# Kernel optimization log

Measured on AMD Instinct MI355X. Metric: run time of the kernel, lower is better.

## Reference

```python
import jax, jax.numpy as jnp
import numpy as np

N = 32768        # tokens (batch*seq)
D = 1024         # input_dim
E = 64           # n_experts
TOPK = 2


def setup_inputs() -> dict:
    key = jax.random.key(0)
    k_x, k_w, k_b, k_wn, k_bn = jax.random.split(key, 5)
    scale = 1.0 / np.sqrt(D)
    return {
        "x": jax.random.normal(k_x, (N, D), dtype=jnp.float32),
        "W": jax.random.uniform(k_w, (D, E), minval=-scale, maxval=scale, dtype=jnp.float32),
        "b": jax.random.uniform(k_b, (E,), minval=-scale, maxval=scale, dtype=jnp.float32),
        "W_noise": jax.random.uniform(k_wn, (D, E), minval=-scale, maxval=scale, dtype=jnp.float32),
        "b_noise": jax.random.uniform(k_bn, (E,), minval=-scale, maxval=scale, dtype=jnp.float32),
    }


def reference(x, W, b, W_noise, b_noise):
    # logits = fc(x): single Linear (router_hidden_dims=[])
    logits = x @ W + b                      # [N, E]
    # training=False (default): no noise path; fc_noise params unused
    topk_logits, topk_indices = jax.lax.top_k(logits, TOPK)  # [N, k]
    # scatter topk logits into a -inf tensor, then softmax
    mask = jnp.sum(jax.nn.one_hot(topk_indices, E, dtype=jnp.bool_), axis=-2)  # [N, E]
    sparse_logits = jnp.where(mask, logits, -jnp.inf)
    routing_probs = jax.nn.softmax(sparse_logits, axis=-1)  # zeros off-topk
    return routing_probs, topk_indices
```

## Files before the change

kernel.cpp:

```cpp
#include <hip/hip_runtime.h>
#include <cstdint>
#include <cstddef>

#define N_TOK 32768
#define DIM   1024
#define NE    64
#define BM    64
#define BK    32
#define NTILES (DIM / BK)

__device__ __forceinline__ void gload16(const float* g, float* l) {
  __builtin_amdgcn_global_load_lds(
      (const __attribute__((address_space(1))) uint32_t*)g,
      (__attribute__((address_space(3))) uint32_t*)l, 16, 0, 0);
}

__global__ __launch_bounds__(256, 2) void router_kernel(
    const float* __restrict__ x, const float* __restrict__ W,
    const float* __restrict__ bias, float* __restrict__ probs,
    float* __restrict__ idxo) {
  __shared__ __align__(1024) float lds[2][4096];

  const int tid  = threadIdx.x;
  const int lane = tid & 63;
  const int wv   = __builtin_amdgcn_readfirstlane(tid >> 6);
  const int tx   = tid & 15;
  const int ty   = tid >> 4;
  const int r0   = blockIdx.x * BM;

  auto stage = [&](int t, int b) {
    const int d0 = t * BK;
    float* xl = &lds[b][0];
    float* wl = &lds[b][2048];
#pragma unroll
    for (int q = 0; q < 2; ++q) {
      const int s = (wv * 2 + q) * 64 + lane;
      gload16(W + (size_t)d0 * NE + (size_t)s * 4, wl + (wv * 2 + q) * 256);
      const int row = s >> 3;
      const int g   = s & 7;
      gload16(x + (size_t)(r0 + row) * DIM + d0 + ((g ^ (row & 7)) << 2),
              xl + (wv * 2 + q) * 256);
    }
  };

  float4 acc[4];
#pragma unroll
  for (int i = 0; i < 4; ++i) acc[i] = make_float4(0.f, 0.f, 0.f, 0.f);

  stage(0, 0);

  for (int t = 0; t < NTILES; ++t) {
    const int b = t & 1;
    __syncthreads();
    if (t + 1 < NTILES) stage(t + 1, (t + 1) & 1);

    const float* wl = &lds[b][2048];
    uintptr_t xb[4];
#pragma unroll
    for (int i = 0; i < 4; ++i) {
      const int r = 4 * ty + i;
      xb[i] = (uintptr_t)(&lds[b][0]) + (uintptr_t)r * (BK * 4) + (uintptr_t)((r & 7) << 4);
    }

#pragma unroll
    for (int q = 0; q < 8; ++q) {
      float4 a0 = *(const float4*)(xb[0] ^ (uintptr_t)(q << 4));
      float4 a1 = *(const float4*)(xb[1] ^ (uintptr_t)(q << 4));
      float4 a2 = *(const float4*)(xb[2] ^ (uintptr_t)(q << 4));
      float4 a3 = *(const float4*)(xb[3] ^ (uintptr_t)(q << 4));
      float4 b0 = *(const float4*)(wl + (q * 4 + 0) * NE + tx * 4);
      float4 b1 = *(const float4*)(wl + (q * 4 + 1) * NE + tx * 4);
      float4 b2 = *(const float4*)(wl + (q * 4 + 2) * NE + tx * 4);
      float4 b3 = *(const float4*)(wl + (q * 4 + 3) * NE + tx * 4);

#define ROWFMA(ACC, A)                                                        \
      ACC.x = fmaf(A.x, b0.x, ACC.x); ACC.y = fmaf(A.x, b0.y, ACC.y);         \
      ACC.z = fmaf(A.x, b0.z, ACC.z); ACC.w = fmaf(A.x, b0.w, ACC.w);         \
      ACC.x = fmaf(A.y, b1.x, ACC.x); ACC.y = fmaf(A.y, b1.y, ACC.y);         \
      ACC.z = fmaf(A.y, b1.z, ACC.z); ACC.w = fmaf(A.y, b1.w, ACC.w);         \
      ACC.x = fmaf(A.z, b2.x, ACC.x); ACC.y = fmaf(A.z, b2.y, ACC.y);         \
      ACC.z = fmaf(A.z, b2.z, ACC.z); ACC.w = fmaf(A.z, b2.w, ACC.w);         \
      ACC.x = fmaf(A.w, b3.x, ACC.x); ACC.y = fmaf(A.w, b3.y, ACC.y);         \
      ACC.z = fmaf(A.w, b3.z, ACC.z); ACC.w = fmaf(A.w, b3.w, ACC.w);

      ROWFMA(acc[0], a0)
      ROWFMA(acc[1], a1)
      ROWFMA(acc[2], a2)
      ROWFMA(acc[3], a3)
#undef ROWFMA
    }
  }

  const float4 bv = *(const float4*)(bias + tx * 4);
#pragma unroll
  for (int i = 0; i < 4; ++i) {
    float4 l = acc[i];
    l.x += bv.x; l.y += bv.y; l.z += bv.z; l.w += bv.w;

    float v1, v2; int j1, j2;
    if (l.y > l.x) { v1 = l.y; j1 = 1; v2 = l.x; j2 = 0; }
    else           { v1 = l.x; j1 = 0; v2 = l.y; j2 = 1; }
    if (l.z > v1)      { v2 = v1; j2 = j1; v1 = l.z; j1 = 2; }
    else if (l.z > v2) { v2 = l.z; j2 = 2; }
    if (l.w > v1)      { v2 = v1; j2 = j1; v1 = l.w; j1 = 3; }
    else if (l.w > v2) { v2 = l.w; j2 = 3; }
    j1 += tx * 4; j2 += tx * 4;

#pragma unroll
    for (int m = 8; m >= 1; m >>= 1) {
      float u1 = __shfl_xor(v1, m, 64);
      int   k1 = __shfl_xor(j1, m, 64);
      float u2 = __shfl_xor(v2, m, 64);
      int   k2 = __shfl_xor(j2, m, 64);
      bool firstWins = (u1 > v1) || (u1 == v1 && k1 < j1);
      if (firstWins) {
        bool u2b = (u2 > v1) || (u2 == v1 && k2 < j1);
        v2 = u2b ? u2 : v1; j2 = u2b ? k2 : j1;
        v1 = u1; j1 = k1;
      } else if ((u1 > v2) || (u1 == v2 && k1 < j2)) {
        v2 = u1; j2 = k1;
      }
    }

    const float e2v = __expf(v2 - v1);
    const float inv = 1.0f / (1.0f + e2v);
    const float p1 = inv, p2 = e2v * inv;

    const int row = r0 + 4 * ty + i;
    const int e0  = tx * 4;
    float4 o;
    o.x = (e0 + 0 == j1) ? p1 : (e0 + 0 == j2) ? p2 : 0.0f;
    o.y = (e0 + 1 == j1) ? p1 : (e0 + 1 == j2) ? p2 : 0.0f;
    o.z = (e0 + 2 == j1) ? p1 : (e0 + 2 == j2) ? p2 : 0.0f;
    o.w = (e0 + 3 == j1) ? p1 : (e0 + 3 == j2) ? p2 : 0.0f;
    *(float4*)(probs + (size_t)row * NE + e0) = o;

    if (tx == 0) {
      float2 oi; oi.x = (float)j1; oi.y = (float)j2;
      *(float2*)(idxo + (size_t)row * 2) = oi;
    }
  }
}

extern "C" void kernel_launch(void* const* d_in, const int* in_sizes, int n_in,
                              void* d_out, int out_size, void* d_ws, size_t ws_size,
                              hipStream_t stream) {
  (void)in_sizes; (void)n_in; (void)out_size; (void)d_ws; (void)ws_size;
  const float* x = (const float*)d_in[0];
  const float* W = (const float*)d_in[1];
  const float* b = (const float*)d_in[2];
  float* out  = (float*)d_out;
  float* idxo = out + (size_t)N_TOK * NE;

  dim3 grid(N_TOK / BM);
  dim3 block(256);
  hipLaunchKernelGGL(router_kernel, grid, block, 0, stream, x, W, b, out, idxo);
}
```

Before: 254.2 us.

## Split K across wave halves, read W via scalar loads, reduce partials in LDS

```diff
diff --git a/kernel.cpp b/kernel.cpp
--- a/kernel.cpp
+++ b/kernel.cpp
@@ -5,9 +5,10 @@
 #define N_TOK 32768
 #define DIM   1024
 #define NE    64
-#define BM    64
-#define BK    32
-#define NTILES (DIM / BK)
+#define RPB   64
+#define KHALF 512
+#define CHUNK 32
+#define NCHUNK (KHALF / CHUNK)
 
 __device__ __forceinline__ void gload16(const float* g, float* l) {
   __builtin_amdgcn_global_load_lds(
@@ -15,129 +16,131 @@
       (__attribute__((address_space(3))) uint32_t*)l, 16, 0, 0);
 }
 
-__global__ __launch_bounds__(256, 2) void router_kernel(
+__global__ __launch_bounds__(512, 4) void router_kernel(
     const float* __restrict__ x, const float* __restrict__ W,
     const float* __restrict__ bias, float* __restrict__ probs,
     float* __restrict__ idxo) {
-  __shared__ __align__(1024) float lds[2][4096];
+  __shared__ __align__(1024) float xs[2][2][RPB][CHUNK];
+  __shared__ float  red[4][RPB][16];
+  __shared__ float4 ex[4][RPB];
+  __shared__ float4 ex2[RPB];
 
   const int tid  = threadIdx.x;
   const int lane = tid & 63;
-  const int wv   = __builtin_amdgcn_readfirstlane(tid >> 6);
-  const int tx   = tid & 15;
-  const int ty   = tid >> 4;
-  const int r0   = blockIdx.x * BM;
+  const int w    = __builtin_amdgcn_readfirstlane(tid >> 6);
+  const int g    = w & 3;
+  const int h    = w >> 2;
+  const int r0   = blockIdx.x * RPB;
 
-  auto stage = [&](int t, int b) {
-    const int d0 = t * BK;
-    float* xl = &lds[b][0];
-    float* wl = &lds[b][2048];
+  auto stage = [&](int cc) {
+    const int buf = cc & 1;
+    float* base = &xs[h][buf][0][0];
+    const int k0 = h * KHALF + cc * CHUNK;
 #pragma unroll
-    for (int q = 0; q < 2; ++q) {
-      const int s = (wv * 2 + q) * 64 + lane;
-      gload16(W + (size_t)d0 * NE + (size_t)s * 4, wl + (wv * 2 + q) * 256);
-      const int row = s >> 3;
-      const int g   = s & 7;
-      gload16(x + (size_t)(r0 + row) * DIM + d0 + ((g ^ (row & 7)) << 2),
-              xl + (wv * 2 + q) * 256);
+    for (int jj = 0; jj < 2; ++jj) {
+      const int j = 2 * g + jj;
+      const int row = 8 * j + (lane >> 3);
+      const int sq  = (lane & 7) ^ (lane >> 3);
+      gload16(x + (size_t)(r0 + row) * DIM + k0 + (sq << 2),
+              base + j * 256);
     }
   };
 
-  float4 acc[4];
+  float acc[16];
 #pragma unroll
-  for (int i = 0; i < 4; ++i) acc[i] = make_float4(0.f, 0.f, 0.f, 0.f);
+  for (int e = 0; e < 16; ++e) acc[e] = 0.0f;
 
-  stage(0, 0);
+  stage(0);
 
-  for (int t = 0; t < NTILES; ++t) {
-    const int b = t & 1;
+  for (int cc = 0; cc < NCHUNK; ++cc) {
     __syncthreads();
-    if (t + 1 < NTILES) stage(t + 1, (t + 1) & 1);
+    if (cc + 1 < NCHUNK) stage(cc + 1);
 
-    const float* wl = &lds[b][2048];
-    uintptr_t xb[4];
+    const int buf = cc & 1;
+    const float* xb = &xs[h][buf][0][0] + lane * CHUNK;
+    const float* Wc = W + (size_t)(h * KHALF + cc * CHUNK) * NE + g * 16;
+
+    float4 xq = make_float4(0.f, 0.f, 0.f, 0.f);
 #pragma unroll
-    for (int i = 0; i < 4; ++i) {
-      const int r = 4 * ty + i;
-      xb[i] = (uintptr_t)(&lds[b][0]) + (uintptr_t)r * (BK * 4) + (uintptr_t)((r & 7) << 4);
-    }
-
+    for (int kk = 0; kk < CHUNK; ++kk) {
+      if ((kk & 3) == 0) {
+        const int slot = (kk >> 2) ^ (lane & 7);
+        xq = *(const float4*)(xb + (slot << 2));
+      }
+      const float xc = ((kk & 3) == 0) ? xq.x
+                     : ((kk & 3) == 1) ? xq.y
+                     : ((kk & 3) == 2) ? xq.z : xq.w;
+      const float* Wk = Wc + (size_t)kk * NE;
 #pragma unroll
-    for (int q = 0; q < 8; ++q) {
-      float4 a0 = *(const float4*)(xb[0] ^ (uintptr_t)(q << 4));
-      float4 a1 = *(const float4*)(xb[1] ^ (uintptr_t)(q << 4));
-      float4 a2 = *(const float4*)(xb[2] ^ (uintptr_t)(q << 4));
-      float4 a3 = *(const float4*)(xb[3] ^ (uintptr_t)(q << 4));
-      float4 b0 = *(const float4*)(wl + (q * 4 + 0) * NE + tx * 4);
-      float4 b1 = *(const float4*)(wl + (q * 4 + 1) * NE + tx * 4);
-      float4 b2 = *(const float4*)(wl + (q * 4 + 2) * NE + tx * 4);
-      float4 b3 = *(const float4*)(wl + (q * 4 + 3) * NE + tx * 4);
-
-#define ROWFMA(ACC, A)                                                        \
-      ACC.x = fmaf(A.x, b0.x, ACC.x); ACC.y = fmaf(A.x, b0.y, ACC.y);         \
-      ACC.z = fmaf(A.x, b0.z, ACC.z); ACC.w = fmaf(A.x, b0.w, ACC.w);         \
-      ACC.x = fmaf(A.y, b1.x, ACC.x); ACC.y = fmaf(A.y, b1.y, ACC.y);         \
-      ACC.z = fmaf(A.y, b1.z, ACC.z); ACC.w = fmaf(A.y, b1.w, ACC.w);         \
-      ACC.x = fmaf(A.z, b2.x, ACC.x); ACC.y = fmaf(A.z, b2.y, ACC.y);         \
-      ACC.z = fmaf(A.z, b2.z, ACC.z); ACC.w = fmaf(A.z, b2.w, ACC.w);         \
-      ACC.x = fmaf(A.w, b3.x, ACC.x); ACC.y = fmaf(A.w, b3.y, ACC.y);         \
-      ACC.z = fmaf(A.w, b3.z, ACC.z); ACC.w = fmaf(A.w, b3.w, ACC.w);
-
-      ROWFMA(acc[0], a0)
-      ROWFMA(acc[1], a1)
-      ROWFMA(acc[2], a2)
-      ROWFMA(acc[3], a3)
-#undef ROWFMA
+      for (int e = 0; e < 16; ++e)
+        acc[e] = fmaf(Wk[e], xc, acc[e]);
     }
   }
 
-  const float4 bv = *(const float4*)(bias + tx * 4);
+  __syncthreads();
+  if (h == 1) {
 #pragma unroll
-  for (int i = 0; i < 4; ++i) {
-    float4 l = acc[i];
-    l.x += bv.x; l.y += bv.y; l.z += bv.z; l.w += bv.w;
+    for (int q = 0; q < 4; ++q)
+      *(float4*)&red[g][lane][q * 4] = make_float4(acc[q*4+0], acc[q*4+1],
+                                                   acc[q*4+2], acc[q*4+3]);
+  }
+  __syncthreads();
+
+  if (h == 0) {
+#pragma unroll
+    for (int q = 0; q < 4; ++q) {
+      float4 r = *(const float4*)&red[g][lane][q * 4];
+      acc[q*4+0] += r.x; acc[q*4+1] += r.y; acc[q*4+2] += r.z; acc[q*4+3] += r.w;
+    }
+#pragma unroll
+    for (int e = 0; e < 16; ++e) acc[e] += bias[g * 16 + e];
 
     float v1, v2; int j1, j2;
-    if (l.y > l.x) { v1 = l.y; j1 = 1; v2 = l.x; j2 = 0; }
-    else           { v1 = l.x; j1 = 0; v2 = l.y; j2 = 1; }
-    if (l.z > v1)      { v2 = v1; j2 = j1; v1 = l.z; j1 = 2; }
-    else if (l.z > v2) { v2 = l.z; j2 = 2; }
-    if (l.w > v1)      { v2 = v1; j2 = j1; v1 = l.w; j1 = 3; }
-    else if (l.w > v2) { v2 = l.w; j2 = 3; }
-    j1 += tx * 4; j2 += tx * 4;
+    if (acc[1] > acc[0]) { v1 = acc[1]; j1 = 1; v2 = acc[0]; j2 = 0; }
+    else                 { v1 = acc[0]; j1 = 0; v2 = acc[1]; j2 = 1; }
+#pragma unroll
+    for (int e = 2; e < 16; ++e) {
+      if (acc[e] > v1)      { v2 = v1; j2 = j1; v1 = acc[e]; j1 = e; }
+      else if (acc[e] > v2) { v2 = acc[e]; j2 = e; }
+    }
+    ex[g][lane] = make_float4(v1, v2, (float)(g * 16 + j1), (float)(g * 16 + j2));
+  }
+  __syncthreads();
 
+  if (w == 0) {
+    float4 m = ex[0][lane];
+    float V1 = m.x, V2 = m.y, J1 = m.z, J2 = m.w;
 #pragma unroll
-    for (int m = 8; m >= 1; m >>= 1) {
-      float u1 = __shfl_xor(v1, m, 64);
-      int   k1 = __shfl_xor(j1, m, 64);
-      float u2 = __shfl_xor(v2, m, 64);
-      int   k2 = __shfl_xor(j2, m, 64);
-      bool firstWins = (u1 > v1) || (u1 == v1 && k1 < j1);
-      if (firstWins) {
-        bool u2b = (u2 > v1) || (u2 == v1 && k2 < j1);
-        v2 = u2b ? u2 : v1; j2 = u2b ? k2 : j1;
-        v1 = u1; j1 = k1;
-      } else if ((u1 > v2) || (u1 == v2 && k1 < j2)) {
-        v2 = u1; j2 = k1;
-      }
+    for (int gg = 1; gg < 4; ++gg) {
+      float4 u = ex[gg][lane];
+      if (u.x > V1) {
+        bool s = (u.y > V1);
+        V2 = s ? u.y : V1; J2 = s ? u.w : J1;
+        V1 = u.x; J1 = u.z;
+      } else if (u.x > V2) { V2 = u.x; J2 = u.z; }
     }
+    const float e2 = __expf(V2 - V1);
+    const float p1 = 1.0f / (1.0f + e2);
+    const float p2 = e2 * p1;
+    ex2[lane] = make_float4(J1, J2, p1, p2);
+    float2 oi; oi.x = J1; oi.y = J2;
+    *(float2*)(idxo + (size_t)(r0 + lane) * 2) = oi;
+  }
+  __syncthreads();
 
-    const float e2v = __expf(v2 - v1);
-    const float inv = 1.0f / (1.0f + e2v);
-    const float p1 = inv, p2 = e2v * inv;
-
-    const int row = r0 + 4 * ty + i;
-    const int e0  = tx * 4;
-    float4 o;
-    o.x = (e0 + 0 == j1) ? p1 : (e0 + 0 == j2) ? p2 : 0.0f;
-    o.y = (e0 + 1 == j1) ? p1 : (e0 + 1 == j2) ? p2 : 0.0f;
-    o.z = (e0 + 2 == j1) ? p1 : (e0 + 2 == j2) ? p2 : 0.0f;
-    o.w = (e0 + 3 == j1) ? p1 : (e0 + 3 == j2) ? p2 : 0.0f;
-    *(float4*)(probs + (size_t)row * NE + e0) = o;
-
-    if (tx == 0) {
-      float2 oi; oi.x = (float)j1; oi.y = (float)j2;
-      *(float2*)(idxo + (size_t)row * 2) = oi;
+  if (h == 0) {
+    float4 f = ex2[lane];
+    const int ij1 = (int)f.x, ij2 = (int)f.y;
+    float* op = probs + (size_t)(r0 + lane) * NE + g * 16;
+#pragma unroll
+    for (int q = 0; q < 4; ++q) {
+      float4 o;
+      const int e0 = g * 16 + q * 4;
+      o.x = (e0 + 0 == ij1) ? f.z : (e0 + 0 == ij2) ? f.w : 0.0f;
+      o.y = (e0 + 1 == ij1) ? f.z : (e0 + 1 == ij2) ? f.w : 0.0f;
+      o.z = (e0 + 2 == ij1) ? f.z : (e0 + 2 == ij2) ? f.w : 0.0f;
+      o.w = (e0 + 3 == ij1) ? f.z : (e0 + 3 == ij2) ? f.w : 0.0f;
+      *(float4*)(op + q * 4) = o;
     }
   }
 }
@@ -152,7 +155,7 @@
   float* out  = (float*)d_out;
   float* idxo = out + (size_t)N_TOK * NE;
 
-  dim3 grid(N_TOK / BM);
-  dim3 block(256);
+  dim3 grid(N_TOK / RPB);
+  dim3 block(512);
   hipLaunchKernelGGL(router_kernel, grid, block, 0, stream, x, W, b, out, idxo);
 }
```

Measured after the change: 248.6 us. 1.02x faster.
